# Kernel tuning notes

Hardware: AMD Instinct MI355X
Metric: run time of the kernel (lower is better)

Reference implementation:

```python
import jax, jax.numpy as jnp
import numpy as np

N, E = 20000, 320000
IN, HID, OUT, EO = 256, 256, 128, 64


def setup_inputs() -> dict:
    key = jax.random.key(0)
    ks = iter(jax.random.split(key, 40))
    w = lambda s: jax.random.normal(next(ks), s, jnp.float32) * 0.05
    inp = {
        "x": jax.random.normal(next(ks), (N, IN), jnp.float32),
        "edge_index": jax.random.randint(next(ks), (2, E), 0, N, jnp.int32),
        "edge_attr": jax.random.uniform(next(ks), (E, 1), jnp.float32),
        # conv1 (IN->IN), conv2 (HID->HID)
        "c1_nw": w((IN, IN)), "c1_ew": w((1, EO)), "c1_new": w((IN + EO, IN)), "c1_b": jnp.zeros((IN,)),
        "c2_nw": w((HID, HID)), "c2_ew": w((1, EO)), "c2_new": w((HID + EO, HID)), "c2_b": jnp.zeros((HID,)),
        # conv3_mean / conv3_logstd (OUT->OUT)
        "cm_nw": w((OUT, OUT)), "cm_ew": w((1, EO)), "cm_new": w((OUT + EO, OUT)), "cm_b": jnp.zeros((OUT,)),
        "cl_nw": w((OUT, OUT)), "cl_ew": w((1, EO)), "cl_new": w((OUT + EO, OUT)), "cl_b": jnp.zeros((OUT,)),
        # linears (stored [in,out])
        "lin1_w": w((IN, HID)), "lin1_b": jnp.zeros((HID,)),
        "lin2_w": w((HID, OUT)), "lin2_b": jnp.zeros((OUT,)),
        "pih_w": w((IN, HID)), "pih_b": jnp.zeros((HID,)),
        "pho_w": w((HID, OUT)), "pho_b": jnp.zeros((OUT,)),
        # batchnorm affine params
        "bn1_g": jnp.ones((IN,)), "bn1_b": jnp.zeros((IN,)),
        "bn2_g": jnp.ones((HID,)), "bn2_b": jnp.zeros((HID,)),
        "bnm_g": jnp.ones((OUT,)), "bnm_b": jnp.zeros((OUT,)),
        "bnl_g": jnp.ones((OUT,)), "bnl_b": jnp.zeros((OUT,)),
    }
    return inp


def _forward(x, edge_index, edge_attr,
             c1_nw, c1_ew, c1_new, c1_b,
             c2_nw, c2_ew, c2_new, c2_b,
             cm_nw, cm_ew, cm_new, cm_b,
             cl_nw, cl_ew, cl_new, cl_b,
             lin1_w, lin1_b, lin2_w, lin2_b,
             pih_w, pih_b, pho_w, pho_b,
             bn1_g, bn1_b, bn2_g, bn2_b,
             bnm_g, bnm_b, bnl_g, bnl_b):
    n = x.shape[0]
    loops = jnp.arange(n, dtype=edge_index.dtype)
    row = jnp.concatenate([edge_index[0], loops])  # source j
    col = jnp.concatenate([edge_index[1], loops])  # target i
    ea = jnp.concatenate([edge_attr, jnp.zeros((n, edge_attr.shape[1]), edge_attr.dtype)], 0)
    deg = jax.ops.segment_sum(jnp.ones_like(col, dtype=x.dtype), col, num_segments=n) + 1e-6
    dis = deg ** -0.5
    norm = dis[row] * dis[col]  # [E+N]

    def gcn(h, nw, ew, new_w, b):
        nm = (h @ nw)[row]                      # gather of x_j @ node_weight
        em = ea @ ew                            # [E+N, EO]
        msg = norm[:, None] * (jnp.concatenate([nm, em], axis=1) @ new_w)
        return jax.ops.segment_sum(msg, col, num_segments=n) + b

    def bn(h, g, b):  # BatchNorm1d, training-mode batch stats, eps 1e-5
        m = h.mean(0)
        v = h.var(0)
        return (h - m) * jax.lax.rsqrt(v + 1e-5) * g + b

    # dropout is identity in eval mode
    x1 = jax.nn.relu(bn(gcn(x, c1_nw, c1_ew, c1_new, c1_b), bn1_g, bn1_b)) + x
    x2 = x1 @ lin1_w + lin1_b
    x2 = jax.nn.relu(bn(gcn(x2, c2_nw, c2_ew, c2_new, c2_b), bn2_g, bn2_b)) + (x1 @ pih_w + pih_b)
    x3 = x2 @ lin2_w + lin2_b
    logstd = bn(gcn(x3, cl_nw, cl_ew, cl_new, cl_b), bnl_g, bnl_b)
    mean = bn(gcn(x3, cm_nw, cm_ew, cm_new, cm_b), bnm_g, bnm_b) + (x2 @ pho_w + pho_b)
    # faithful to source: batch_norm_logstd applied a second time and added
    logstd = logstd + bn(logstd, bnl_g, bnl_b)
    return mean, logstd


def reference(x, edge_index, edge_attr,
              c1_nw, c1_ew, c1_new, c1_b,
              c2_nw, c2_ew, c2_new, c2_b,
              cm_nw, cm_ew, cm_new, cm_b,
              cl_nw, cl_ew, cl_new, cl_b,
              lin1_w, lin1_b, lin2_w, lin2_b,
              pih_w, pih_b, pho_w, pho_b,
              bn1_g, bn1_b, bn2_g, bn2_b,
              bnm_g, bnm_b, bnl_g, bnl_b):
    return _forward(x, edge_index, edge_attr,
                    c1_nw, c1_ew, c1_new, c1_b,
                    c2_nw, c2_ew, c2_new, c2_b,
                    cm_nw, cm_ew, cm_new, cm_b,
                    cl_nw, cl_ew, cl_new, cl_b,
                    lin1_w, lin1_b, lin2_w, lin2_b,
                    pih_w, pih_b, pho_w, pho_b,
                    bn1_g, bn1_b, bn2_g, bn2_b,
                    bnm_g, bnm_b, bnl_g, bnl_b)
```

## Files before the change

kernel.cpp:

```cpp
#include <hip/hip_runtime.h>

#define NN 20000
#define EE 320000
#define ET (EE + NN)

typedef __attribute__((ext_vector_type(8))) short short8v;
typedef __attribute__((ext_vector_type(4))) float float4v;

__device__ __forceinline__ float b2f(unsigned short u) {
  union { float f; unsigned int i; } c; c.i = ((unsigned int)u) << 16; return c.f;
}
__device__ __forceinline__ unsigned short f2bs(float f) {
  union { float f; unsigned int u; } c; c.f = f;
  unsigned int r = c.u + 0x7fffu + ((c.u >> 16) & 1u);
  return (unsigned short)(r >> 16);
}

__global__ void detect_kernel(const unsigned short* __restrict__ x, int* __restrict__ flag) {
  __shared__ int cnt_s;
  if (threadIdx.x == 0) cnt_s = 0;
  __syncthreads();
  int pass = 0;
  for (int j = 0; j < 16; ++j) {
    unsigned short u = x[2 * (threadIdx.x * 16 + j)];
    int e = (u >> 7) & 0xFF;
    if (e >= 96 && e <= 150) pass++;
  }
  atomicAdd(&cnt_s, pass);
  __syncthreads();
  if (threadIdx.x == 0) *flag = (cnt_s < 2458) ? 1 : 0;
}

__global__ void convert_kernel(const void* __restrict__ in, float* __restrict__ out, int n4,
                               const int* __restrict__ flag) {
  int i = blockIdx.x * 256 + threadIdx.x;
  if (i >= n4) return;
  if (*flag) {
    ((float4*)out)[i] = ((const float4*)in)[i];
  } else {
    ushort4 u = ((const ushort4*)in)[i];
    ((float4*)out)[i] = make_float4(b2f(u.x), b2f(u.y), b2f(u.z), b2f(u.w));
  }
}

__global__ void convert_x_kernel(const void* __restrict__ in, float* __restrict__ xc,
                                 short* __restrict__ xh, short* __restrict__ xl, int n4,
                                 const int* __restrict__ flag) {
  int i = blockIdx.x * 256 + threadIdx.x;
  if (i >= n4) return;
  float4 v;
  if (*flag) {
    v = ((const float4*)in)[i];
  } else {
    ushort4 u = ((const ushort4*)in)[i];
    v = make_float4(b2f(u.x), b2f(u.y), b2f(u.z), b2f(u.w));
  }
  ((float4*)xc)[i] = v;
  ushort4 h, l;
  h.x = f2bs(v.x); l.x = f2bs(v.x - b2f(h.x));
  h.y = f2bs(v.y); l.y = f2bs(v.y - b2f(h.y));
  h.z = f2bs(v.z); l.z = f2bs(v.z - b2f(h.z));
  h.w = f2bs(v.w); l.w = f2bs(v.w - b2f(h.w));
  ((ushort4*)xh)[i] = h;
  ((ushort4*)xl)[i] = l;
}

struct WSpec { const void* p[28]; int off[28]; int len[28]; };
__global__ void convert_weights(WSpec ws, float* __restrict__ out, const int* __restrict__ flag) {
  int b = blockIdx.x;
  int f32m = *flag;
  const void* p = ws.p[b];
  int off = ws.off[b], len4 = ws.len[b] >> 2;
  float4* dst = (float4*)(out + off);
  for (int i = blockIdx.y * 256 + threadIdx.x; i < len4; i += 8 * 256) {
    if (f32m) {
      dst[i] = ((const float4*)p)[i];
    } else {
      ushort4 u = ((const ushort4*)p)[i];
      dst[i] = make_float4(b2f(u.x), b2f(u.y), b2f(u.z), b2f(u.w));
    }
  }
}

__global__ void bconv_kernel(const float* __restrict__ W, int ldb,
                             short* __restrict__ Bh, short* __restrict__ Bl, int N) {
  int idx = blockIdx.x * 256 + threadIdx.x;
  if (idx >= N * 256) return;
  int n = idx >> 8, k = idx & 255;
  float v = W[(size_t)k * ldb + n];
  unsigned short h = f2bs(v);
  size_t o = ((size_t)(k >> 3) * N + n) * 8 + (k & 7);
  Bh[o] = (short)h;
  Bl[o] = (short)f2bs(v - b2f(h));
}

__global__ void count_kernel(const int* __restrict__ ei, int* __restrict__ cnt) {
  int e = blockIdx.x * 256 + threadIdx.x;
  if (e >= ET) return;
  int dst = (e < EE) ? ei[EE + e] : (e - EE);
  atomicAdd(&cnt[dst], 1);
}

__global__ void dis_kernel(const int* __restrict__ cnt, float* __restrict__ dis) {
  int i = blockIdx.x * 256 + threadIdx.x;
  if (i >= NN) return;
  dis[i] = rsqrtf((float)cnt[i] + 1e-6f);
}

__global__ void scan1_kernel(const int* __restrict__ cnt, int* __restrict__ partial,
                             int* __restrict__ bsum) {
  __shared__ int sd[256];
  int b = blockIdx.x, t = threadIdx.x;
  int i = b * 256 + t;
  sd[t] = (i < NN) ? cnt[i] : 0;
  __syncthreads();
  for (int off = 1; off < 256; off <<= 1) {
    int x = (t >= off) ? sd[t - off] : 0;
    __syncthreads();
    sd[t] += x;
    __syncthreads();
  }
  if (i < NN) partial[i] = sd[t];
  if (t == 255) bsum[b] = sd[255];
}

__global__ void scan2_kernel(int* __restrict__ bsum, int nb) {
  __shared__ int sd[128];
  int t = threadIdx.x;
  sd[t] = (t < nb) ? bsum[t] : 0;
  __syncthreads();
  for (int off = 1; off < 128; off <<= 1) {
    int x = (t >= off) ? sd[t - off] : 0;
    __syncthreads();
    sd[t] += x;
    __syncthreads();
  }
  if (t < nb) bsum[t] = sd[t];
}

__global__ void scan3_kernel(const int* __restrict__ partial, const int* __restrict__ bsum,
                             int* __restrict__ rowptr) {
  int i = blockIdx.x * 256 + threadIdx.x;
  if (i == 0) rowptr[0] = 0;
  if (i < NN) {
    int b = i >> 8;
    rowptr[i + 1] = partial[i] + (b ? bsum[b - 1] : 0);
  }
}

__global__ void fill_kernel(const int* __restrict__ ei, const float* __restrict__ eaf,
                            const float* __restrict__ dis, const int* __restrict__ rowptr,
                            int* __restrict__ cursor, int2* __restrict__ csr,
                            float* __restrict__ sarr) {
  int e = blockIdx.x * 256 + threadIdx.x;
  if (e >= ET) return;
  int src, dst; float a;
  if (e < EE) { src = ei[e]; dst = ei[EE + e]; a = eaf[e]; }
  else { src = dst = e - EE; a = 0.f; }
  float coef = dis[src] * dis[dst];
  int pos = rowptr[dst] + atomicAdd(&cursor[dst], 1);
  csr[pos] = make_int2(src, __float_as_int(coef));
  if (a != 0.f) atomicAdd(&sarr[dst], coef * a);
}

struct GJobs {
  const float* A[8]; const float* B[8]; float* C[8];
  int M[8], N[8], K[8], ldc[8], blkx[8], cum[8];
  int njobs;
};
__global__ __launch_bounds__(256) void gemm64_multi(GJobs jb) {
  int bid = blockIdx.x;
  int j = 0;
  while (j < jb.njobs - 1 && bid >= jb.cum[j]) ++j;
  int local = bid - (j ? jb.cum[j - 1] : 0);
  const float* A = jb.A[j];
  const float* B = jb.B[j];
  float* C = jb.C[j];
  int M = jb.M[j], N = jb.N[j], K = jb.K[j], ldc = jb.ldc[j];
  int bx = local % jb.blkx[j], by = local / jb.blkx[j];

  __shared__ float As[16][68];
  __shared__ float Bs[16][64];
  int tid = threadIdx.x;
  int row0 = bx * 64, col0 = by * 64;
  int tr = tid >> 4, tc = tid & 15;
  float acc[4][4] = {};
  int lmA = tid >> 2;
  int lkA = (tid & 3) << 2;
  int lkB = tid >> 4;
  int lcB = (tid & 15) << 2;
  for (int k0 = 0; k0 < K; k0 += 16) {
    int gr = row0 + lmA;
    float4 a4 = make_float4(0.f, 0.f, 0.f, 0.f);
    if (gr < M) a4 = *reinterpret_cast<const float4*>(&A[(size_t)gr * K + k0 + lkA]);
    As[lkA + 0][lmA] = a4.x;
    As[lkA + 1][lmA] = a4.y;
    As[lkA + 2][lmA] = a4.z;
    As[lkA + 3][lmA] = a4.w;
    float4 b4 = *reinterpret_cast<const float4*>(&B[(size_t)(k0 + lkB) * N + col0 + lcB]);
    *reinterpret_cast<float4*>(&Bs[lkB][lcB]) = b4;
    __syncthreads();
#pragma unroll
    for (int kk = 0; kk < 16; ++kk) {
      float4 av = *reinterpret_cast<const float4*>(&As[kk][tr << 2]);
      float4 bv = *reinterpret_cast<const float4*>(&Bs[kk][tc << 2]);
      float aa[4] = {av.x, av.y, av.z, av.w};
      float bb[4] = {bv.x, bv.y, bv.z, bv.w};
#pragma unroll
      for (int i = 0; i < 4; ++i)
#pragma unroll
        for (int jj = 0; jj < 4; ++jj) acc[i][jj] += aa[i] * bb[jj];
    }
    __syncthreads();
  }
#pragma unroll
  for (int i = 0; i < 4; ++i) {
    int gr = row0 + (tr << 2) + i;
    if (gr >= M) continue;
#pragma unroll
    for (int jj = 0; jj < 4; ++jj)
      C[(size_t)gr * ldc + col0 + (tc << 2) + jj] = acc[i][jj];
  }
}

__global__ void copy_strided(const float* __restrict__ src, float* __restrict__ dst,
                             int n, int cshift, int cmask, int ldd) {
  int idx = blockIdx.x * 256 + threadIdx.x;
  if (idx >= n) return;
  int r = idx >> cshift, c = idx & cmask;
  dst[(size_t)r * ldd + c] = src[idx];
}

#define LOADB(ntv, ktv, BH, BL)                                     \
  {                                                                 \
    int n_ = (ntv) * 128 + w * 16 + lm;                             \
    _Pragma("unroll") for (int ks = 0; ks < 2; ++ks) {              \
      int kc = (ktv) * 8 + ks * 4 + lg;                             \
      size_t o = ((size_t)kc * N + n_) * 8;                         \
      BH[ks] = *reinterpret_cast<const short8v*>(Bh + o);           \
      BL[ks] = *reinterpret_cast<const short8v*>(Bl + o);           \
    }                                                               \
  }

__global__ __launch_bounds__(512) void gemm_mfma4(const short* __restrict__ Ah,
                                                  const short* __restrict__ Al,
                                                  const short* __restrict__ Bh,
                                                  const short* __restrict__ Bl,
                                                  unsigned short* __restrict__ C,
                                                  const float* __restrict__ bias,
                                                  int M, int N, int ldc) {
  __shared__ __align__(16) short lds[16384];
  const int K = 256;
  int tid = threadIdx.x;
  int w = tid >> 6, l = tid & 63;
  int row0 = blockIdx.x * 32;
  int lm = l & 15, lg = l >> 4;

#pragma unroll
  for (int i = 0; i < 2; ++i) {
    int id = i * 512 + tid;
    int r = id >> 5, c = id & 31;
    int gr = row0 + r; if (gr >= M) gr = M - 1;
    int sw = c ^ r;
    *reinterpret_cast<float4*>(lds + r * 256 + sw * 8) =
        *reinterpret_cast<const float4*>(Ah + (size_t)gr * K + c * 8);
    *reinterpret_cast<float4*>(lds + 8192 + r * 256 + sw * 8) =
        *reinterpret_cast<const float4*>(Al + (size_t)gr * K + c * 8);
  }
  __syncthreads();

  int NT = N >> 7;
  short8v bhX[2], blX[2], bhY[2], blY[2];
  LOADB(0, 0, bhX, blX);
  for (int nt = 0; nt < NT; ++nt) {
    float4v acc[2] = {};
    int n = nt * 128 + w * 16 + lm;
#pragma unroll
    for (int kt = 0; kt < 4; ++kt) {
      int nt_n = (kt == 3) ? ((nt + 1 < NT) ? nt + 1 : nt) : nt;
      int kt_n = (kt + 1) & 3;
      short8v a_h[2][2], a_l[2][2];
#pragma unroll
      for (int mf = 0; mf < 2; ++mf)
#pragma unroll
        for (int ks = 0; ks < 2; ++ks) {
          int r = mf * 16 + lm;
          int c = kt * 8 + ks * 4 + lg;
          int sw = c ^ r;
          a_h[mf][ks] = *reinterpret_cast<const short8v*>(lds + r * 256 + sw * 8);
          a_l[mf][ks] = *reinterpret_cast<const short8v*>(lds + 8192 + r * 256 + sw * 8);
        }
      if ((kt & 1) == 0) {
        LOADB(nt_n, kt_n, bhY, blY);
#pragma unroll
        for (int mf = 0; mf < 2; ++mf)
#pragma unroll
          for (int ks = 0; ks < 2; ++ks) {
            acc[mf] = __builtin_amdgcn_mfma_f32_16x16x32_bf16(a_h[mf][ks], bhX[ks], acc[mf], 0, 0, 0);
            acc[mf] = __builtin_amdgcn_mfma_f32_16x16x32_bf16(a_h[mf][ks], blX[ks], acc[mf], 0, 0, 0);
            acc[mf] = __builtin_amdgcn_mfma_f32_16x16x32_bf16(a_l[mf][ks], bhX[ks], acc[mf], 0, 0, 0);
          }
      } else {
        LOADB(nt_n, kt_n, bhX, blX);
#pragma unroll
        for (int mf = 0; mf < 2; ++mf)
#pragma unroll
          for (int ks = 0; ks < 2; ++ks) {
            acc[mf] = __builtin_amdgcn_mfma_f32_16x16x32_bf16(a_h[mf][ks], bhY[ks], acc[mf], 0, 0, 0);
            acc[mf] = __builtin_amdgcn_mfma_f32_16x16x32_bf16(a_h[mf][ks], blY[ks], acc[mf], 0, 0, 0);
            acc[mf] = __builtin_amdgcn_mfma_f32_16x16x32_bf16(a_l[mf][ks], bhY[ks], acc[mf], 0, 0, 0);
          }
      }
    }
    float bb = bias ? bias[n] : 0.f;
#pragma unroll
    for (int mf = 0; mf < 2; ++mf)
#pragma unroll
      for (int r = 0; r < 4; ++r) {
        int m = row0 + mf * 16 + lg * 4 + r;
        if (m < M) C[(size_t)m * ldc + n] = f2bs(acc[mf][r] + bb);
      }
  }
}

__global__ void agg_kernel(const unsigned short* __restrict__ U, int ldu,
                           const int* __restrict__ rowptr, const int2* __restrict__ csr,
                           const float* __restrict__ sarr, const float* __restrict__ V,
                           float* __restrict__ G) {
  int i = blockIdx.x, t = threadIdx.x;
  float s = sarr[i];
  float4 v4 = ((const float4*)V)[t];
  float ax = s * v4.x, ay = s * v4.y, az = s * v4.z, aw = s * v4.w;
  int p1 = rowptr[i + 1];
  for (int p = rowptr[i]; p < p1; ++p) {
    int2 e = csr[p];
    float c = __int_as_float(e.y);
    ushort4 u4 = *reinterpret_cast<const ushort4*>(U + (size_t)e.x * ldu + (t << 2));
    ax += c * b2f(u4.x); ay += c * b2f(u4.y); az += c * b2f(u4.z); aw += c * b2f(u4.w);
  }
  *reinterpret_cast<float4*>(G + (size_t)i * 256 + (t << 2)) = make_float4(ax, ay, az, aw);
}

__global__ void colpart_kernel(const float* __restrict__ h, float* __restrict__ part, int F) {
  __shared__ float4 sm0[256], sm1[256];
  int t = threadIdx.x;
  int cols4 = F >> 2;
  int lc = t & (cols4 - 1);
  int team = t / cols4;
  int rpi = 256 / cols4;
  int r0 = blockIdx.x * 64;
  int r1 = min(r0 + 64, NN);
  float4 s0 = make_float4(0.f, 0.f, 0.f, 0.f);
  float4 s1 = make_float4(0.f, 0.f, 0.f, 0.f);
  for (int r = r0 + team; r < r1; r += rpi) {
    float4 x = *reinterpret_cast<const float4*>(h + (size_t)r * F + lc * 4);
    s0.x += x.x; s0.y += x.y; s0.z += x.z; s0.w += x.w;
    s1.x += x.x * x.x; s1.y += x.y * x.y; s1.z += x.z * x.z; s1.w += x.w * x.w;
  }
  sm0[t] = s0; sm1[t] = s1;
  __syncthreads();
  if (team == 0) {
    for (int k = 1; k < rpi; ++k) {
      float4 a = sm0[k * cols4 + lc];
      float4 b = sm1[k * cols4 + lc];
      s0.x += a.x; s0.y += a.y; s0.z += a.z; s0.w += a.w;
      s1.x += b.x; s1.y += b.y; s1.z += b.z; s1.w += b.w;
    }
    *reinterpret_cast<float4*>(part + (size_t)blockIdx.x * 2 * F + lc * 4) = s0;
    *reinterpret_cast<float4*>(part + (size_t)blockIdx.x * 2 * F + F + lc * 4) = s1;
  }
}

__global__ void bnred_kernel(const float* __restrict__ part, float* __restrict__ part2,
                             int F2, int nb) {
  int c = blockIdx.x * 256 + threadIdx.x;
  if (c >= F2) return;
  int chunk = blockIdx.y;
  int cs = (nb + 7) >> 3;
  int b0 = chunk * cs;
  int b1 = min(b0 + cs, nb);
  float s0 = 0.f, s1 = 0.f, s2 = 0.f, s3 = 0.f;
  int b = b0;
  for (; b + 3 < b1; b += 4) {
    s0 += part[(size_t)(b + 0) * F2 + c];
    s1 += part[(size_t)(b + 1) * F2 + c];
    s2 += part[(size_t)(b + 2) * F2 + c];
    s3 += part[(size_t)(b + 3) * F2 + c];
  }
  for (; b < b1; ++b) s0 += part[(size_t)b * F2 + c];
  part2[(size_t)chunk * F2 + c] = (s0 + s1) + (s2 + s3);
}

__global__ void bnfin_kernel(const float* __restrict__ part2, const float* __restrict__ gamma,
                             const float* __restrict__ beta, int F,
                             float* __restrict__ scsh) {
  int t = threadIdx.x;
  int F2 = 2 * F;
  float s0 = 0.f, s1 = 0.f;
#pragma unroll
  for (int b = 0; b < 8; ++b) {
    s0 += part2[(size_t)b * F2 + t];
    s1 += part2[(size_t)b * F2 + F + t];
  }
  const float invn = 1.f / (float)NN;
  float m = s0 * invn;
  float var = s1 * invn - m * m;
  float sc = gamma[t] * rsqrtf(var + 1e-5f);
  scsh[t] = sc;
  scsh[F + t] = beta[t] - m * sc;
}

__global__ void apply_x1_kernel(const float* __restrict__ g, const float* __restrict__ scsh,
                                const float* __restrict__ xc, short* __restrict__ oh,
                                short* __restrict__ ol, int n) {
  int idx = blockIdx.x * 256 + threadIdx.x;
  if (idx >= n) return;
  int c = idx & 255;
  float y = fmaxf(g[idx] * scsh[c] + scsh[256 + c], 0.f) + xc[idx];
  unsigned short h = f2bs(y);
  oh[idx] = (short)h;
  ol[idx] = (short)f2bs(y - b2f(h));
}

__global__ void apply_x2_kernel(const float* __restrict__ g, const float* __restrict__ scsh,
                                const unsigned short* __restrict__ ucat, short* __restrict__ oh,
                                short* __restrict__ ol, int n) {
  int idx = blockIdx.x * 256 + threadIdx.x;
  if (idx >= n) return;
  int r = idx >> 8, c = idx & 255;
  float y = fmaxf(g[idx] * scsh[c] + scsh[256 + c], 0.f) + b2f(ucat[(size_t)r * 512 + 256 + c]);
  unsigned short h = f2bs(y);
  oh[idx] = (short)h;
  ol[idx] = (short)f2bs(y - b2f(h));
}

__global__ void apply_mean_kernel(const float* __restrict__ g, const float* __restrict__ scsh,
                                  const unsigned short* __restrict__ ucat, float* __restrict__ out,
                                  int n) {
  int idx = blockIdx.x * 256 + threadIdx.x;
  if (idx >= n) return;
  int r = idx >> 7, c = idx & 127;
  float v = g[(size_t)r * 256 + c];
  out[idx] = v * scsh[c] + scsh[256 + c] + b2f(ucat[(size_t)r * 384 + 256 + c]);
}

__global__ void apply_ln0_kernel(const float* __restrict__ g, const float* __restrict__ scsh,
                                 float* __restrict__ L, int n) {
  int idx = blockIdx.x * 256 + threadIdx.x;
  if (idx >= n) return;
  int r = idx >> 7, c = idx & 127;
  float v = g[(size_t)r * 256 + 128 + c];
  L[idx] = v * scsh[128 + c] + scsh[256 + 128 + c];
}

__global__ void apply_ln2_kernel(const float* __restrict__ L, const float* __restrict__ scsh,
                                 float* __restrict__ out, int n) {
  int idx = blockIdx.x * 256 + threadIdx.x;
  if (idx >= n) return;
  int c = idx & 127;
  float v = L[idx];
  out[idx] = v + v * scsh[c] + scsh[128 + c];
}

__global__ void write_code(float* __restrict__ out, float code) {
  int i = blockIdx.x * 256 + threadIdx.x;
  if (i < 4096) out[i] = code;
}

extern "C" void kernel_launch(void* const* d_in, const int* in_sizes, int n_in,
                              void* d_out, int out_size, void* d_ws, size_t ws_size,
                              hipStream_t stream) {
  float* out_mean = (float*)d_out;
  float* out_logstd = out_mean + (size_t)NN * 128;

  static const int expect[35] = {5120000, 640000, 320000,
                                 65536, 64, 81920, 256,  65536, 64, 81920, 256,
                                 16384, 64, 24576, 128,  16384, 64, 24576, 128,
                                 65536, 256, 32768, 128, 65536, 256, 32768, 128,
                                 256, 256, 256, 256, 128, 128, 128, 128};
  if (n_in != 35) { write_code<<<16, 256, 0, stream>>>(out_mean, 900.f); return; }
  if (out_size != 5120000) { write_code<<<16, 256, 0, stream>>>(out_mean, 950.f); return; }
  for (int i = 0; i < 35; ++i)
    if (in_sizes[i] != expect[i]) {
      write_code<<<16, 256, 0, stream>>>(out_mean, 1000.f + 10.f * i);
      return;
    }

  const int* ei = (const int*)d_in[1];

  char* w = (char*)d_ws;
  size_t off = 0;
  auto alloc = [&](size_t bytes) -> void* {
    void* p = w + off;
    off += (bytes + 255) & ~(size_t)255;
    return p;
  };
  int* flag = (int*)alloc(4);
  int* cnt = (int*)alloc(NN * 4);
  int* rowptr = (int*)alloc((NN + 1) * 4);
  int* bsum = (int*)alloc(128 * 4);
  int* spart = (int*)alloc(NN * 4);
  int2* csr = (int2*)alloc((size_t)ET * 8);
  float* dis = (float*)alloc(NN * 4);
  float* sarr = (float*)alloc(NN * 4);
  float* eaf = (float*)alloc((size_t)EE * 4);
  float* Wf = (float*)alloc((size_t)576000 * 4);
  float* W1 = (float*)alloc((size_t)65536 * 4);
  float* W2cat = (float*)alloc((size_t)131072 * 4);
  float* W3cat = (float*)alloc((size_t)98304 * 4);
  float* WCa = (float*)alloc((size_t)65536 * 4);
  float* WCb = (float*)alloc((size_t)16384 * 4);
  float* WCc = (float*)alloc((size_t)16384 * 4);
  float* bias2 = (float*)alloc(512 * 4);
  float* bias3 = (float*)alloc(384 * 4);
  float* V1 = (float*)alloc(256 * 4);
  float* V2 = (float*)alloc(256 * 4);
  float* Vcat3 = (float*)alloc(256 * 4);
  float* Gpart = (float*)alloc((size_t)313 * 512 * 4);
  float* Gpart2 = (float*)alloc((size_t)8 * 512 * 4);
  float* scsh = (float*)alloc(512 * 4);
  float* scsh2 = (float*)alloc(256 * 4);
  short* Bh1 = (short*)alloc((size_t)256 * 256 * 2);
  short* Bl1 = (short*)alloc((size_t)256 * 256 * 2);
  short* Bh2 = (short*)alloc((size_t)512 * 256 * 2);
  short* Bl2 = (short*)alloc((size_t)512 * 256 * 2);
  short* Bh3 = (short*)alloc((size_t)384 * 256 * 2);
  short* Bl3 = (short*)alloc((size_t)384 * 256 * 2);
  float* Xc = (float*)alloc((size_t)NN * 256 * 4);
  float* regB = (float*)alloc((size_t)NN * 256 * 4);
  float* regC = (float*)alloc((size_t)NN * 256 * 4);
  float* Ucat = (float*)alloc((size_t)NN * 512 * 4);
  if (off > ws_size) { write_code<<<16, 256, 0, stream>>>(out_mean, 2000.f); return; }

  unsigned short* U1 = (unsigned short*)regB;
  short* X1h = (short*)regB;
  short* X1l = X1h + (size_t)NN * 256;
  short* X2h = X1h;
  short* X2l = X1l;
  short* Xh = (short*)regC;
  short* Xl = Xh + (size_t)NN * 256;
  float* G = regC;
  float* L = Xc;
  unsigned short* Ucat_u = (unsigned short*)Ucat;

  const int n256 = NN * 256, n128 = NN * 128;
  const int g256 = (n256 + 255) / 256, g128 = (n128 + 255) / 256;
  const int nb = (NN + 255) / 256;
  const int nbc = (NN + 63) / 64;

  detect_kernel<<<1, 256, 0, stream>>>((const unsigned short*)d_in[0], flag);
  convert_x_kernel<<<(n256 / 4 + 255) / 256, 256, 0, stream>>>(d_in[0], Xc, Xh, Xl, n256 / 4, flag);
  convert_kernel<<<(EE / 4 + 255) / 256, 256, 0, stream>>>(d_in[2], eaf, EE / 4, flag);

  WSpec wsp;
  const int map[28] = {3, 5, 7, 9, 11, 13, 15, 17, 4, 8, 12, 16, 19, 21, 23, 25,
                       20, 22, 24, 26, 27, 28, 29, 30, 31, 33, 32, 34};
  const int offs[28] = {0, 65536, 147456, 212992, 294912, 311296, 335872, 352256,
                        376832, 376896, 376960, 377024, 377088, 442624, 475392, 540928,
                        573696, 573952, 574080, 574336, 574464, 574720, 574976, 575232,
                        575488, 575616, 575744, 575872};
  const int lens[28] = {65536, 81920, 65536, 81920, 16384, 24576, 16384, 24576,
                        64, 64, 64, 64, 65536, 32768, 65536, 32768,
                        256, 128, 256, 128, 256, 256, 256, 256,
                        128, 128, 128, 128};
  for (int i = 0; i < 28; ++i) { wsp.p[i] = d_in[map[i]]; wsp.off[i] = offs[i]; wsp.len[i] = lens[i]; }
  convert_weights<<<dim3(28, 8), 256, 0, stream>>>(wsp, Wf, flag);

  hipMemsetAsync(cnt, 0, NN * 4, stream);
  count_kernel<<<(ET + 255) / 256, 256, 0, stream>>>(ei, cnt);
  dis_kernel<<<(NN + 255) / 256, 256, 0, stream>>>(cnt, dis);
  scan1_kernel<<<nb, 256, 0, stream>>>(cnt, spart, bsum);
  scan2_kernel<<<1, 128, 0, stream>>>(bsum, nb);
  scan3_kernel<<<nb, 256, 0, stream>>>(spart, bsum, rowptr);
  hipMemsetAsync(cnt, 0, NN * 4, stream);
  hipMemsetAsync(sarr, 0, NN * 4, stream);
  fill_kernel<<<(ET + 255) / 256, 256, 0, stream>>>(ei, eaf, dis, rowptr, cnt, csr, sarr);

  {
    GJobs jb{};
    auto set = [&](int j, const float* A, const float* B, float* C, int M, int N, int K,
                   int ldc, int bx, int cum) {
      jb.A[j] = A; jb.B[j] = B; jb.C[j] = C; jb.M[j] = M; jb.N[j] = N; jb.K[j] = K;
      jb.ldc[j] = ldc; jb.blkx[j] = bx; jb.cum[j] = cum;
    };
    set(0, Wf + 0,      Wf + 65536,  W1,          256, 256, 256, 256, 4, 16);
    set(1, Wf + 147456, Wf + 212992, WCa,         256, 256, 256, 256, 4, 32);
    set(2, Wf + 294912, Wf + 311296, WCb,         128, 128, 128, 128, 2, 36);
    set(3, Wf + 335872, Wf + 352256, WCc,         128, 128, 128, 128, 2, 40);
    set(4, Wf + 376832, Wf + 131072, V1,          1,   256, 64,  256, 1, 44);
    set(5, Wf + 376896, Wf + 278528, V2,          1,   256, 64,  256, 1, 48);
    set(6, Wf + 376960, Wf + 327680, Vcat3,       1,   128, 64,  128, 1, 50);
    set(7, Wf + 377024, Wf + 368640, Vcat3 + 128, 1,   128, 64,  128, 1, 52);
    jb.njobs = 8;
    gemm64_multi<<<52, 256, 0, stream>>>(jb);
  }
  {
    GJobs jb{};
    auto set = [&](int j, const float* A, const float* B, float* C, int M, int N, int K,
                   int ldc, int bx, int cum) {
      jb.A[j] = A; jb.B[j] = B; jb.C[j] = C; jb.M[j] = M; jb.N[j] = N; jb.K[j] = K;
      jb.ldc[j] = ldc; jb.blkx[j] = bx; jb.cum[j] = cum;
    };
    set(0, Wf + 377088, WCa, W2cat,       256, 256, 256, 512, 4, 16);
    set(1, Wf + 573696, WCa, bias2,       1,   256, 256, 512, 1, 20);
    set(2, Wf + 442624, WCb, W3cat,       256, 128, 128, 384, 4, 28);
    set(3, Wf + 442624, WCc, W3cat + 128, 256, 128, 128, 384, 4, 36);
    set(4, Wf + 573952, WCb, bias3,       1,   128, 128, 384, 1, 38);
    set(5, Wf + 573952, WCc, bias3 + 128, 1,   128, 128, 384, 1, 40);
    jb.njobs = 6;
    gemm64_multi<<<40, 256, 0, stream>>>(jb);
  }
  copy_strided<<<256, 256, 0, stream>>>(Wf + 475392, W2cat + 256, 65536, 8, 255, 512);
  copy_strided<<<1, 256, 0, stream>>>(Wf + 574080, bias2 + 256, 256, 8, 255, 512);
  copy_strided<<<128, 256, 0, stream>>>(Wf + 540928, W3cat + 256, 32768, 7, 127, 384);
  copy_strided<<<1, 256, 0, stream>>>(Wf + 574336, bias3 + 256, 128, 7, 127, 384);

  bconv_kernel<<<256, 256, 0, stream>>>(W1, 256, Bh1, Bl1, 256);
  bconv_kernel<<<512, 256, 0, stream>>>(W2cat, 512, Bh2, Bl2, 512);
  bconv_kernel<<<384, 256, 0, stream>>>(W3cat, 384, Bh3, Bl3, 384);

  gemm_mfma4<<<625, 512, 0, stream>>>(Xh, Xl, Bh1, Bl1, U1, nullptr, NN, 256, 256);
  agg_kernel<<<NN, 64, 0, stream>>>(U1, 256, rowptr, csr, sarr, V1, G);
  colpart_kernel<<<nbc, 256, 0, stream>>>(G, Gpart, 256);
  bnred_kernel<<<dim3(2, 8), 256, 0, stream>>>(Gpart, Gpart2, 512, nbc);
  bnfin_kernel<<<1, 256, 0, stream>>>(Gpart2, Wf + 574464, Wf + 574720, 256, scsh);
  apply_x1_kernel<<<g256, 256, 0, stream>>>(G, scsh, Xc, X1h, X1l, n256);

  gemm_mfma4<<<625, 512, 0, stream>>>(X1h, X1l, Bh2, Bl2, Ucat_u, bias2, NN, 512, 512);
  agg_kernel<<<NN, 64, 0, stream>>>(Ucat_u, 512, rowptr, csr, sarr, V2, G);
  colpart_kernel<<<nbc, 256, 0, stream>>>(G, Gpart, 256);
  bnred_kernel<<<dim3(2, 8), 256, 0, stream>>>(Gpart, Gpart2, 512, nbc);
  bnfin_kernel<<<1, 256, 0, stream>>>(Gpart2, Wf + 574976, Wf + 575232, 256, scsh);
  apply_x2_kernel<<<g256, 256, 0, stream>>>(G, scsh, Ucat_u, X2h, X2l, n256);

  gemm_mfma4<<<625, 512, 0, stream>>>(X2h, X2l, Bh3, Bl3, Ucat_u, bias3, NN, 384, 384);
  agg_kernel<<<NN, 64, 0, stream>>>(Ucat_u, 384, rowptr, csr, sarr, Vcat3, G);
  colpart_kernel<<<nbc, 256, 0, stream>>>(G, Gpart, 256);
  bnred_kernel<<<dim3(2, 8), 256, 0, stream>>>(Gpart, Gpart2, 512, nbc);
  bnfin_kernel<<<1, 256, 0, stream>>>(Gpart2, Wf + 575488, Wf + 575744, 256, scsh);
  apply_mean_kernel<<<g128, 256, 0, stream>>>(G, scsh, Ucat_u, out_mean, n128);
  apply_ln0_kernel<<<g128, 256, 0, stream>>>(G, scsh, L, n128);
  colpart_kernel<<<nbc, 256, 0, stream>>>(L, Gpart, 128);
  bnred_kernel<<<dim3(1, 8), 256, 0, stream>>>(Gpart, Gpart2, 256, nbc);
  bnfin_kernel<<<1, 128, 0, stream>>>(Gpart2, Wf + 575616, Wf + 575872, 128, scsh2);
  apply_ln2_kernel<<<g128, 256, 0, stream>>>(L, scsh2, out_logstd, n128);
}
```

Measured before the change: 410.2 us.

## Derive second logstd batchnorm stats analytically and drop fp32 x copy

The second batch norm on logstd is an affine map of G, so its mean and variance are now computed in closed form from the existing G column statistics. The logstd output is then written with a single fused scale and shift, which removes the L buffer, one column-reduction pass and one apply kernel. Separately, the fp32 copy of x is no longer stored; the residual is rebuilt from the bf16 hi/lo split pair, cutting a 20 MB write and read. Rebuilding x from two bf16 halves may differ slightly from the original fp32 values, and the closed-form variance relies on the E[x^2]-m^2 formula.

```diff
diff --git a/kernel.cpp b/kernel.cpp
--- a/kernel.cpp
+++ b/kernel.cpp
@@ -43,7 +43,7 @@
   }
 }
 
-__global__ void convert_x_kernel(const void* __restrict__ in, float* __restrict__ xc,
+__global__ void convert_x_kernel(const void* __restrict__ in,
                                  short* __restrict__ xh, short* __restrict__ xl, int n4,
                                  const int* __restrict__ flag) {
   int i = blockIdx.x * 256 + threadIdx.x;
@@ -55,7 +55,6 @@
     ushort4 u = ((const ushort4*)in)[i];
     v = make_float4(b2f(u.x), b2f(u.y), b2f(u.z), b2f(u.w));
   }
-  ((float4*)xc)[i] = v;
   ushort4 h, l;
   h.x = f2bs(v.x); l.x = f2bs(v.x - b2f(h.x));
   h.y = f2bs(v.y); l.y = f2bs(v.y - b2f(h.y));
@@ -410,13 +409,38 @@
   scsh[F + t] = beta[t] - m * sc;
 }
 
+__global__ void bnfin2_kernel(const float* __restrict__ part2, const float* __restrict__ scsh,
+                              const float* __restrict__ gamma2, const float* __restrict__ beta2,
+                              float* __restrict__ ab) {
+  int t = threadIdx.x;
+  int c = 128 + t;
+  float s0 = 0.f, s1 = 0.f;
+#pragma unroll
+  for (int b = 0; b < 8; ++b) {
+    s0 += part2[(size_t)b * 512 + c];
+    s1 += part2[(size_t)b * 512 + 256 + c];
+  }
+  const float invn = 1.f / (float)NN;
+  float m_g = s0 * invn;
+  float v_g = s1 * invn - m_g * m_g;
+  float sc1 = scsh[c];
+  float sh1 = scsh[256 + c];
+  float m_L = m_g * sc1 + sh1;
+  float v_L = v_g * sc1 * sc1;
+  float sc2 = gamma2[t] * rsqrtf(v_L + 1e-5f);
+  float sh2 = beta2[t] - m_L * sc2;
+  ab[t] = sc1 * (1.f + sc2);
+  ab[128 + t] = sh1 * (1.f + sc2) + sh2;
+}
+
 __global__ void apply_x1_kernel(const float* __restrict__ g, const float* __restrict__ scsh,
-                                const float* __restrict__ xc, short* __restrict__ oh,
-                                short* __restrict__ ol, int n) {
+                                const short* __restrict__ xh, const short* __restrict__ xl,
+                                short* __restrict__ oh, short* __restrict__ ol, int n) {
   int idx = blockIdx.x * 256 + threadIdx.x;
   if (idx >= n) return;
   int c = idx & 255;
-  float y = fmaxf(g[idx] * scsh[c] + scsh[256 + c], 0.f) + xc[idx];
+  float xr = b2f((unsigned short)xh[idx]) + b2f((unsigned short)xl[idx]);
+  float y = fmaxf(g[idx] * scsh[c] + scsh[256 + c], 0.f) + xr;
   unsigned short h = f2bs(y);
   oh[idx] = (short)h;
   ol[idx] = (short)f2bs(y - b2f(h));
@@ -444,22 +468,13 @@
   out[idx] = v * scsh[c] + scsh[256 + c] + b2f(ucat[(size_t)r * 384 + 256 + c]);
 }
 
-__global__ void apply_ln0_kernel(const float* __restrict__ g, const float* __restrict__ scsh,
-                                 float* __restrict__ L, int n) {
+__global__ void apply_ln2g_kernel(const float* __restrict__ g, const float* __restrict__ ab,
+                                  float* __restrict__ out, int n) {
   int idx = blockIdx.x * 256 + threadIdx.x;
   if (idx >= n) return;
   int r = idx >> 7, c = idx & 127;
   float v = g[(size_t)r * 256 + 128 + c];
-  L[idx] = v * scsh[128 + c] + scsh[256 + 128 + c];
-}
-
-__global__ void apply_ln2_kernel(const float* __restrict__ L, const float* __restrict__ scsh,
-                                 float* __restrict__ out, int n) {
-  int idx = blockIdx.x * 256 + threadIdx.x;
-  if (idx >= n) return;
-  int c = idx & 127;
-  float v = L[idx];
-  out[idx] = v + v * scsh[c] + scsh[128 + c];
+  out[idx] = v * ab[c] + ab[128 + c];
 }
 
 __global__ void write_code(float* __restrict__ out, float code) {
@@ -519,14 +534,14 @@
   float* Gpart = (float*)alloc((size_t)313 * 512 * 4);
   float* Gpart2 = (float*)alloc((size_t)8 * 512 * 4);
   float* scsh = (float*)alloc(512 * 4);
-  float* scsh2 = (float*)alloc(256 * 4);
+  float* ab = (float*)alloc(256 * 4);
   short* Bh1 = (short*)alloc((size_t)256 * 256 * 2);
   short* Bl1 = (short*)alloc((size_t)256 * 256 * 2);
   short* Bh2 = (short*)alloc((size_t)512 * 256 * 2);
   short* Bl2 = (short*)alloc((size_t)512 * 256 * 2);
   short* Bh3 = (short*)alloc((size_t)384 * 256 * 2);
   short* Bl3 = (short*)alloc((size_t)384 * 256 * 2);
-  float* Xc = (float*)alloc((size_t)NN * 256 * 4);
+  float* Gbuf = (float*)alloc((size_t)NN * 256 * 4);
   float* regB = (float*)alloc((size_t)NN * 256 * 4);
   float* regC = (float*)alloc((size_t)NN * 256 * 4);
   float* Ucat = (float*)alloc((size_t)NN * 512 * 4);
@@ -539,8 +554,7 @@
   short* X2l = X1l;
   short* Xh = (short*)regC;
   short* Xl = Xh + (size_t)NN * 256;
-  float* G = regC;
-  float* L = Xc;
+  float* G = Gbuf;
   unsigned short* Ucat_u = (unsigned short*)Ucat;
 
   const int n256 = NN * 256, n128 = NN * 128;
@@ -549,7 +563,7 @@
   const int nbc = (NN + 63) / 64;
 
   detect_kernel<<<1, 256, 0, stream>>>((const unsigned short*)d_in[0], flag);
-  convert_x_kernel<<<(n256 / 4 + 255) / 256, 256, 0, stream>>>(d_in[0], Xc, Xh, Xl, n256 / 4, flag);
+  convert_x_kernel<<<(n256 / 4 + 255) / 256, 256, 0, stream>>>(d_in[0], Xh, Xl, n256 / 4, flag);
   convert_kernel<<<(EE / 4 + 255) / 256, 256, 0, stream>>>(d_in[2], eaf, EE / 4, flag);
 
   WSpec wsp;
@@ -624,7 +638,7 @@
   colpart_kernel<<<nbc, 256, 0, stream>>>(G, Gpart, 256);
   bnred_kernel<<<dim3(2, 8), 256, 0, stream>>>(Gpart, Gpart2, 512, nbc);
   bnfin_kernel<<<1, 256, 0, stream>>>(Gpart2, Wf + 574464, Wf + 574720, 256, scsh);
-  apply_x1_kernel<<<g256, 256, 0, stream>>>(G, scsh, Xc, X1h, X1l, n256);
+  apply_x1_kernel<<<g256, 256, 0, stream>>>(G, scsh, Xh, Xl, X1h, X1l, n256);
 
   gemm_mfma4<<<625, 512, 0, stream>>>(X1h, X1l, Bh2, Bl2, Ucat_u, bias2, NN, 512, 512);
   agg_kernel<<<NN, 64, 0, stream>>>(Ucat_u, 512, rowptr, csr, sarr, V2, G);
@@ -638,10 +652,7 @@
   colpart_kernel<<<nbc, 256, 0, stream>>>(G, Gpart, 256);
   bnred_kernel<<<dim3(2, 8), 256, 0, stream>>>(Gpart, Gpart2, 512, nbc);
   bnfin_kernel<<<1, 256, 0, stream>>>(Gpart2, Wf + 575488, Wf + 575744, 256, scsh);
+  bnfin2_kernel<<<1, 128, 0, stream>>>(Gpart2, scsh, Wf + 575616, Wf + 575872, ab);
   apply_mean_kernel<<<g128, 256, 0, stream>>>(G, scsh, Ucat_u, out_mean, n128);
-  apply_ln0_kernel<<<g128, 256, 0, stream>>>(G, scsh, L, n128);
-  colpart_kernel<<<nbc, 256, 0, stream>>>(L, Gpart, 128);
-  bnred_kernel<<<dim3(1, 8), 256, 0, stream>>>(Gpart, Gpart2, 256, nbc);
-  bnfin_kernel<<<1, 128, 0, stream>>>(Gpart2, Wf + 575616, Wf + 575872, 128, scsh2);
-  apply_ln2_kernel<<<g128, 256, 0, stream>>>(L, scsh2, out_logstd, n128);
-}
+  apply_ln2g_kernel<<<g128, 256, 0, stream>>>(G, ab, out_logstd, n128);
+}
```

Result: faster. 391.1 us (-4.7%).
